# Kernel tuning notes

Measured on AMD Instinct MI355X. Metric: run time of the kernel, lower is better.

The kernel has to match this reference:

```python
import jax, jax.numpy as jnp
import numpy as np

NUM_CONN = 8

def _ein_reduce(f):
    # Einstein t-norm fold over last axis: T(a,b) = ab / (2 - (a+b-ab))
    acc = f[..., 0]
    for i in range(1, f.shape[-1]):
        b = f[..., i]
        ab = acc * b
        acc = ab / (2.0 - (acc + b - ab))
    return acc

def _coein_reduce(f):
    # Einstein t-conorm fold over last axis: S(a,b) = (a+b) / (1 + ab)
    acc = f[..., 0]
    for i in range(1, f.shape[-1]):
        b = f[..., i]
        acc = (acc + b) / (1.0 + acc * b)
    return acc

def _ddlg_layer(x, w, idx, is_train):
    # x: [B, in], idx: [out, C] int, w: [out, 4]
    feats = x[:, idx]                      # [B, out, C] gather
    ops = jnp.stack([
        jnp.min(feats, axis=-1),
        jnp.max(feats, axis=-1),
        _ein_reduce(feats),
        _coein_reduce(feats),
    ], axis=-1)                            # [B, out, 4]
    if is_train:
        prob = jax.nn.softmax(w, axis=-1)  # [out, 4]
    else:
        prob = jax.nn.one_hot(jnp.argmax(w, axis=-1), 4, dtype=x.dtype)
    return jnp.einsum('bof,of->bo', ops, prob)

def setup_inputs() -> dict:
    key = jax.random.key(0)
    ks = jax.random.split(key, 6)
    sizes = [4096, 2048, 1024, 2048, 4096]
    x = jax.random.uniform(ks[0], (4096, sizes[0]), dtype=jnp.float32)
    ws = [jax.random.normal(ks[1 + i], (sizes[i + 1], 4), dtype=jnp.float32) for i in range(4)]
    rng = np.random.default_rng(0)
    idxs = []
    for i in range(4):
        # randperm-without-replacement per output neuron
        perm = np.argsort(rng.random((sizes[i + 1], sizes[i])), axis=-1)[:, :NUM_CONN]
        idxs.append(jnp.asarray(perm, dtype=jnp.int32))
    return {
        'x': x,
        'w0': ws[0], 'w1': ws[1], 'w2': ws[2], 'w3': ws[3],
        'idx0': idxs[0], 'idx1': idxs[1], 'idx2': idxs[2], 'idx3': idxs[3],
        'is_train': 1,
    }

def reference(x, w0, w1, w2, w3, idx0, idx1, idx2, idx3, is_train):
    h = _ddlg_layer(x, w0, idx0, is_train)
    h = _ddlg_layer(h, w1, idx1, is_train)
    h = _ddlg_layer(h, w2, idx2, is_train)
    h = _ddlg_layer(h, w3, idx3, is_train)
    return h
```

## Files before the change

kernel.cpp:

```cpp
#include <hip/hip_runtime.h>


#define BATCH 4096

typedef _Float16 h2 __attribute__((ext_vector_type(2)));

__device__ __forceinline__ float fastrcp(float x) { return __builtin_amdgcn_rcpf(x); }
__device__ __forceinline__ _Float16 hrcp(_Float16 x) {
#if __has_builtin(__builtin_amdgcn_rcph)
    return __builtin_amdgcn_rcph(x);
#else
    return (_Float16)__builtin_amdgcn_rcpf((float)x);
#endif
}
__device__ __forceinline__ h2 splat2(_Float16 s) { h2 v = {s, s}; return v; }

__device__ __forceinline__ void probs_of(const float* __restrict__ w, int o,
                                         bool train, _Float16 P[4]) {
    const float4 wv = ((const float4*)w)[o];
    float v0 = wv.x, v1 = wv.y, v2 = wv.z, v3 = wv.w;
    if (train) {
        float m = fmaxf(fmaxf(v0, v1), fmaxf(v2, v3));
        float e0 = __expf(v0 - m), e1 = __expf(v1 - m);
        float e2 = __expf(v2 - m), e3 = __expf(v3 - m);
        float inv = fastrcp(e0 + e1 + e2 + e3);
        P[0] = (_Float16)(e0 * inv); P[1] = (_Float16)(e1 * inv);
        P[2] = (_Float16)(e2 * inv); P[3] = (_Float16)(e3 * inv);
    } else {
        int a = 0; float best = v0;
        if (v1 > best) { best = v1; a = 1; }
        if (v2 > best) { best = v2; a = 2; }
        if (v3 > best) { best = v3; a = 3; }
        P[0] = (_Float16)(a == 0 ? 1.0f : 0.0f);
        P[1] = (_Float16)(a == 1 ? 1.0f : 0.0f);
        P[2] = (_Float16)(a == 2 ? 1.0f : 0.0f);
        P[3] = (_Float16)(a == 3 ? 1.0f : 0.0f);
    }
}

struct Raw { h2 lo, hi; };

__device__ __forceinline__ Raw row_at(const uint2* __restrict__ rows, int i) {
    const uint2 v = rows[i];
    Raw r;
    r.lo = __builtin_bit_cast(h2, v.x);
    r.hi = __builtin_bit_cast(h2, v.y);
    return r;
}
__device__ __forceinline__ uint2 raw_bits(Raw r) {
    return uint2{__builtin_bit_cast(unsigned, r.lo), __builtin_bit_cast(unsigned, r.hi)};
}

struct Chain { h2 mn0, mn1, mx0, mx1, De0, De1, Ne0, Ne1, Nc0, Nc1, Dc0, Dc1; };

__device__ __forceinline__ void cinit(Chain& C, Raw v) {
    const h2 one = splat2((_Float16)1.0f), two = splat2((_Float16)2.0f);
    C.mn0 = v.lo; C.mx0 = v.lo; C.De0 = v.lo;
    C.Ne0 = two - v.lo; C.Nc0 = one + v.lo; C.Dc0 = one - v.lo;
    C.mn1 = v.hi; C.mx1 = v.hi; C.De1 = v.hi;
    C.Ne1 = two - v.hi; C.Nc1 = one + v.hi; C.Dc1 = one - v.hi;
}
__device__ __forceinline__ void cstep(Chain& C, Raw v) {
    const h2 two = splat2((_Float16)2.0f);
    C.mn0 = __builtin_elementwise_min(C.mn0, v.lo);
    C.mn1 = __builtin_elementwise_min(C.mn1, v.hi);
    C.mx0 = __builtin_elementwise_max(C.mx0, v.lo);
    C.mx1 = __builtin_elementwise_max(C.mx1, v.hi);
    C.De0 *= v.lo;            C.De1 *= v.hi;
    C.Ne0 *= (two - v.lo);    C.Ne1 *= (two - v.hi);
    C.Nc0 += C.Nc0 * v.lo;    C.Nc1 += C.Nc1 * v.hi;
    C.Dc0 -= C.Dc0 * v.lo;    C.Dc1 -= C.Dc1 * v.hi;
}
__device__ __forceinline__ Raw finale(const Chain& C, const _Float16 P[4]) {
    h2 s10 = C.Ne0 + C.De0, s11 = C.Ne1 + C.De1;
    h2 s20 = C.Nc0 + C.Dc0, s21 = C.Nc1 + C.Dc1;
    h2 d10 = C.Nc0 - C.Dc0, d11 = C.Nc1 - C.Dc1;
    h2 ss0 = s10 * s20,     ss1 = s11 * s21;
    h2 r0 = {hrcp(ss0[0]), hrcp(ss0[1])};
    h2 r1 = {hrcp(ss1[0]), hrcp(ss1[1])};
    h2 t10 = (C.De0 + C.De0) * s20, t11 = (C.De1 + C.De1) * s21;
    h2 t20 = d10 * s10,             t21 = d11 * s11;
    const h2 P0 = splat2(P[0]), P1 = splat2(P[1]);
    const h2 P2 = splat2(P[2]), P3 = splat2(P[3]);
    h2 num0 = P2 * t10 + P3 * t20;
    h2 num1 = P2 * t11 + P3 * t21;
    Raw res;
    res.lo = P0 * C.mn0 + P1 * C.mx0 + num0 * r0;
    res.hi = P0 * C.mn1 + P1 * C.mx1 + num1 * r1;
    return res;
}

__device__ __forceinline__ Raw gate(const uint2* __restrict__ rows,
                                    const int4* __restrict__ idx,
                                    const float* __restrict__ w,
                                    bool train, int o) {
    const int4 i0 = idx[o * 2], i1 = idx[o * 2 + 1];
    _Float16 P[4];
    probs_of(w, o, train, P);
    Raw A[8];
    A[0] = row_at(rows, i0.x); A[1] = row_at(rows, i0.y);
    A[2] = row_at(rows, i0.z); A[3] = row_at(rows, i0.w);
    A[4] = row_at(rows, i1.x); A[5] = row_at(rows, i1.y);
    A[6] = row_at(rows, i1.z); A[7] = row_at(rows, i1.w);
    Chain C; cinit(C, A[0]);
#pragma unroll
    for (int c = 1; c < 8; ++c) cstep(C, A[c]);
    return finale(C, P);
}

__global__ __launch_bounds__(512, 6) void ddlg_fused(const float* __restrict__ x,
                                                     const float* __restrict__ w0,
                                                     const float* __restrict__ w1,
                                                     const float* __restrict__ w2,
                                                     const float* __restrict__ w3,
                                                     const int* __restrict__ is_train,
                                                     const int4* __restrict__ idx0,
                                                     const int4* __restrict__ idx1,
                                                     const int4* __restrict__ idx2,
                                                     const int4* __restrict__ idx3,
                                                     float* __restrict__ out) {
    __shared__ __align__(16) _Float16 lds[24576];
    const int t  = threadIdx.x;
    const int b0 = blockIdx.x << 2;
    const bool train = (*is_train) != 0;

    const uint2* xl  = (const uint2*)lds;
    const uint2* h0v = (const uint2*)(lds + 16384);
    const uint2* h1v = (const uint2*)lds;
    const uint2* h2v = (const uint2*)(lds + 16384);

#pragma unroll
    for (int c = 0; c < 8; ++c) {
        const int j = (c << 9) + t;
        const float v0 = x[(size_t)(b0 + 0) * 4096 + j];
        const float v1 = x[(size_t)(b0 + 1) * 4096 + j];
        const float v2 = x[(size_t)(b0 + 2) * 4096 + j];
        const float v3 = x[(size_t)(b0 + 3) * 4096 + j];
        h2 a = {(_Float16)v0, (_Float16)v1};
        h2 b = {(_Float16)v2, (_Float16)v3};
        uint2 hv = {__builtin_bit_cast(unsigned, a), __builtin_bit_cast(unsigned, b)};
        *(uint2*)(lds + (j << 2)) = hv;
    }
    __syncthreads();

#pragma unroll
    for (int k = 0; k < 4; ++k) {
        const int o = (k << 9) + t;
        Raw r = gate(xl, idx0, w0, train, o);
        *(uint2*)(lds + 16384 + (o << 2)) = raw_bits(r);
    }
    __syncthreads();

#pragma unroll
    for (int k = 0; k < 2; ++k) {
        const int o = (k << 9) + t;
        Raw r = gate(h0v, idx1, w1, train, o);
        *(uint2*)(lds + (o << 2)) = raw_bits(r);
    }
    __syncthreads();

#pragma unroll
    for (int k = 0; k < 4; ++k) {
        const int o = (k << 9) + t;
        Raw r = gate(h1v, idx2, w2, train, o);
        *(uint2*)(lds + 16384 + (o << 2)) = raw_bits(r);
    }
    __syncthreads();

#pragma unroll
    for (int k = 0; k < 8; ++k) {
        const int o = (k << 9) + t;
        Raw r = gate(h2v, idx3, w3, train, o);
        out[(size_t)(b0 + 0) * 4096 + o] = (float)r.lo[0];
        out[(size_t)(b0 + 1) * 4096 + o] = (float)r.lo[1];
        out[(size_t)(b0 + 2) * 4096 + o] = (float)r.hi[0];
        out[(size_t)(b0 + 3) * 4096 + o] = (float)r.hi[1];
    }
}

extern "C" void kernel_launch(void* const* d_in, const int* in_sizes, int n_in,
                              void* d_out, int out_size, void* d_ws, size_t ws_size,
                              hipStream_t stream) {
    const float* x        = (const float*)d_in[0];
    const float* w0       = (const float*)d_in[1];
    const float* w1       = (const float*)d_in[2];
    const float* w2       = (const float*)d_in[3];
    const float* w3       = (const float*)d_in[4];
    const int4*  idx0     = (const int4*)d_in[5];
    const int4*  idx1     = (const int4*)d_in[6];
    const int4*  idx2     = (const int4*)d_in[7];
    const int4*  idx3     = (const int4*)d_in[8];
    const int*   is_train = (const int*)d_in[9];
    float*       out      = (float*)d_out;

    (void)d_ws; (void)ws_size;

    ddlg_fused<<<1024, 512, 0, stream>>>(x, w0, w1, w2, w3, is_train,
                                         idx0, idx1, idx2, idx3, out);
}
```

Measured before the change: 167.5 us.

## Double-batch tiles per block with prefetched next input and vectorized IO

Each block now processes eight batch rows as two four-row tiles with 1024 threads. The next tile's input is loaded from global memory during layer 1 and written to LDS during layer 3, so that load latency overlaps compute. Input loads and output stores use float4 vectors, and the softmax drops its max subtraction. The trade-offs are extra registers and barriers, a less stable softmax for large weights, and halved grid size.

New measurement: 352.1 us. 110% more time.

```diff
diff --git a/kernel.cpp b/kernel.cpp
--- a/kernel.cpp
+++ b/kernel.cpp
@@ -1,7 +1,5 @@
 #include <hip/hip_runtime.h>
 
-
-#define BATCH 4096
 
 typedef _Float16 h2 __attribute__((ext_vector_type(2)));
 
@@ -14,23 +12,25 @@
 #endif
 }
 __device__ __forceinline__ h2 splat2(_Float16 s) { h2 v = {s, s}; return v; }
+__device__ __forceinline__ unsigned packh2(float a, float b) {
+    h2 v = {(_Float16)a, (_Float16)b};
+    return __builtin_bit_cast(unsigned, v);
+}
 
 __device__ __forceinline__ void probs_of(const float* __restrict__ w, int o,
                                          bool train, _Float16 P[4]) {
     const float4 wv = ((const float4*)w)[o];
-    float v0 = wv.x, v1 = wv.y, v2 = wv.z, v3 = wv.w;
     if (train) {
-        float m = fmaxf(fmaxf(v0, v1), fmaxf(v2, v3));
-        float e0 = __expf(v0 - m), e1 = __expf(v1 - m);
-        float e2 = __expf(v2 - m), e3 = __expf(v3 - m);
+        float e0 = __expf(wv.x), e1 = __expf(wv.y);
+        float e2 = __expf(wv.z), e3 = __expf(wv.w);
         float inv = fastrcp(e0 + e1 + e2 + e3);
         P[0] = (_Float16)(e0 * inv); P[1] = (_Float16)(e1 * inv);
         P[2] = (_Float16)(e2 * inv); P[3] = (_Float16)(e3 * inv);
     } else {
-        int a = 0; float best = v0;
-        if (v1 > best) { best = v1; a = 1; }
-        if (v2 > best) { best = v2; a = 2; }
-        if (v3 > best) { best = v3; a = 3; }
+        int a = 0; float best = wv.x;
+        if (wv.y > best) { best = wv.y; a = 1; }
+        if (wv.z > best) { best = wv.z; a = 2; }
+        if (wv.w > best) { best = wv.w; a = 3; }
         P[0] = (_Float16)(a == 0 ? 1.0f : 0.0f);
         P[1] = (_Float16)(a == 1 ? 1.0f : 0.0f);
         P[2] = (_Float16)(a == 2 ? 1.0f : 0.0f);
@@ -108,73 +108,99 @@
     return finale(C, P);
 }
 
-__global__ __launch_bounds__(512, 6) void ddlg_fused(const float* __restrict__ x,
-                                                     const float* __restrict__ w0,
-                                                     const float* __restrict__ w1,
-                                                     const float* __restrict__ w2,
-                                                     const float* __restrict__ w3,
-                                                     const int* __restrict__ is_train,
-                                                     const int4* __restrict__ idx0,
-                                                     const int4* __restrict__ idx1,
-                                                     const int4* __restrict__ idx2,
-                                                     const int4* __restrict__ idx3,
-                                                     float* __restrict__ out) {
+__global__ __launch_bounds__(1024, 8) void ddlg_fused(const float* __restrict__ x,
+                                                      const float* __restrict__ w0,
+                                                      const float* __restrict__ w1,
+                                                      const float* __restrict__ w2,
+                                                      const float* __restrict__ w3,
+                                                      const int* __restrict__ is_train,
+                                                      const int4* __restrict__ idx0,
+                                                      const int4* __restrict__ idx1,
+                                                      const int4* __restrict__ idx2,
+                                                      const int4* __restrict__ idx3,
+                                                      float* __restrict__ out) {
     __shared__ __align__(16) _Float16 lds[24576];
     const int t  = threadIdx.x;
-    const int b0 = blockIdx.x << 2;
+    const int b0 = blockIdx.x << 3;
     const bool train = (*is_train) != 0;
+    const int j0 = t << 2;
 
     const uint2* xl  = (const uint2*)lds;
     const uint2* h0v = (const uint2*)(lds + 16384);
     const uint2* h1v = (const uint2*)lds;
     const uint2* h2v = (const uint2*)(lds + 16384);
-
-#pragma unroll
-    for (int c = 0; c < 8; ++c) {
-        const int j = (c << 9) + t;
-        const float v0 = x[(size_t)(b0 + 0) * 4096 + j];
-        const float v1 = x[(size_t)(b0 + 1) * 4096 + j];
-        const float v2 = x[(size_t)(b0 + 2) * 4096 + j];
-        const float v3 = x[(size_t)(b0 + 3) * 4096 + j];
-        h2 a = {(_Float16)v0, (_Float16)v1};
-        h2 b = {(_Float16)v2, (_Float16)v3};
-        uint2 hv = {__builtin_bit_cast(unsigned, a), __builtin_bit_cast(unsigned, b)};
-        *(uint2*)(lds + (j << 2)) = hv;
+    uint2* const h0w = (uint2*)(lds + 16384);
+    uint2* const h1w = (uint2*)lds;
+    uint4* const xlw = (uint4*)lds;
+
+    {
+        const float4 v0 = *(const float4*)(x + (size_t)(b0 + 0) * 4096 + j0);
+        const float4 v1 = *(const float4*)(x + (size_t)(b0 + 1) * 4096 + j0);
+        const float4 v2 = *(const float4*)(x + (size_t)(b0 + 2) * 4096 + j0);
+        const float4 v3 = *(const float4*)(x + (size_t)(b0 + 3) * 4096 + j0);
+        xlw[t * 2]     = uint4{packh2(v0.x, v1.x), packh2(v2.x, v3.x),
+                               packh2(v0.y, v1.y), packh2(v2.y, v3.y)};
+        xlw[t * 2 + 1] = uint4{packh2(v0.z, v1.z), packh2(v2.z, v3.z),
+                               packh2(v0.w, v1.w), packh2(v2.w, v3.w)};
     }
     __syncthreads();
 
+    unsigned pre[8];
+#pragma unroll 1
+    for (int tile = 0; tile < 2; ++tile) {
+        const int bb = b0 + (tile << 2);
+        const bool dopre = (tile == 0);
+
 #pragma unroll
-    for (int k = 0; k < 4; ++k) {
-        const int o = (k << 9) + t;
-        Raw r = gate(xl, idx0, w0, train, o);
-        *(uint2*)(lds + 16384 + (o << 2)) = raw_bits(r);
-    }
-    __syncthreads();
+        for (int k = 0; k < 2; ++k) {
+            const int o = 2 * t + k;
+            h0w[o] = raw_bits(gate(xl, idx0, w0, train, o));
+        }
+        __syncthreads();
+
+        float4 p0, p1, p2, p3;
+        if (dopre) {
+            p0 = *(const float4*)(x + (size_t)(b0 + 4) * 4096 + j0);
+            p1 = *(const float4*)(x + (size_t)(b0 + 5) * 4096 + j0);
+            p2 = *(const float4*)(x + (size_t)(b0 + 6) * 4096 + j0);
+            p3 = *(const float4*)(x + (size_t)(b0 + 7) * 4096 + j0);
+        }
+        h1w[t] = raw_bits(gate(h0v, idx1, w1, train, t));
+        if (dopre) {
+            pre[0] = packh2(p0.x, p1.x); pre[1] = packh2(p2.x, p3.x);
+            pre[2] = packh2(p0.y, p1.y); pre[3] = packh2(p2.y, p3.y);
+            pre[4] = packh2(p0.z, p1.z); pre[5] = packh2(p2.z, p3.z);
+            pre[6] = packh2(p0.w, p1.w); pre[7] = packh2(p2.w, p3.w);
+        }
+        __syncthreads();
 
 #pragma unroll
-    for (int k = 0; k < 2; ++k) {
-        const int o = (k << 9) + t;
-        Raw r = gate(h0v, idx1, w1, train, o);
-        *(uint2*)(lds + (o << 2)) = raw_bits(r);
-    }
-    __syncthreads();
-
-#pragma unroll
-    for (int k = 0; k < 4; ++k) {
-        const int o = (k << 9) + t;
-        Raw r = gate(h1v, idx2, w2, train, o);
-        *(uint2*)(lds + 16384 + (o << 2)) = raw_bits(r);
-    }
-    __syncthreads();
-
-#pragma unroll
-    for (int k = 0; k < 8; ++k) {
-        const int o = (k << 9) + t;
-        Raw r = gate(h2v, idx3, w3, train, o);
-        out[(size_t)(b0 + 0) * 4096 + o] = (float)r.lo[0];
-        out[(size_t)(b0 + 1) * 4096 + o] = (float)r.lo[1];
-        out[(size_t)(b0 + 2) * 4096 + o] = (float)r.hi[0];
-        out[(size_t)(b0 + 3) * 4096 + o] = (float)r.hi[1];
+        for (int k = 0; k < 2; ++k) {
+            const int o = 2 * t + k;
+            h0w[o] = raw_bits(gate(h1v, idx2, w2, train, o));
+        }
+        __syncthreads();
+
+        if (dopre) {
+            xlw[t * 2]     = uint4{pre[0], pre[1], pre[2], pre[3]};
+            xlw[t * 2 + 1] = uint4{pre[4], pre[5], pre[6], pre[7]};
+        }
+        {
+            Raw r0 = gate(h2v, idx3, w3, train, 4 * t);
+            Raw r1 = gate(h2v, idx3, w3, train, 4 * t + 1);
+            Raw r2 = gate(h2v, idx3, w3, train, 4 * t + 2);
+            Raw r3 = gate(h2v, idx3, w3, train, 4 * t + 3);
+            float4 o4;
+            o4 = make_float4((float)r0.lo[0], (float)r1.lo[0], (float)r2.lo[0], (float)r3.lo[0]);
+            *(float4*)(out + (size_t)(bb + 0) * 4096 + j0) = o4;
+            o4 = make_float4((float)r0.lo[1], (float)r1.lo[1], (float)r2.lo[1], (float)r3.lo[1]);
+            *(float4*)(out + (size_t)(bb + 1) * 4096 + j0) = o4;
+            o4 = make_float4((float)r0.hi[0], (float)r1.hi[0], (float)r2.hi[0], (float)r3.hi[0]);
+            *(float4*)(out + (size_t)(bb + 2) * 4096 + j0) = o4;
+            o4 = make_float4((float)r0.hi[1], (float)r1.hi[1], (float)r2.hi[1], (float)r3.hi[1]);
+            *(float4*)(out + (size_t)(bb + 3) * 4096 + j0) = o4;
+        }
+        __syncthreads();
     }
 }
 
@@ -195,6 +221,6 @@
 
     (void)d_ws; (void)ws_size;
 
-    ddlg_fused<<<1024, 512, 0, stream>>>(x, w0, w1, w2, w3, is_train,
+    ddlg_fused<<<512, 1024, 0, stream>>>(x, w0, w1, w2, w3, is_train,
                                          idx0, idx1, idx2, idx3, out);
 }
```
